# Optimization experiments

Measured on AMD Instinct MI355X. Metric: run time of the kernel, lower is better.

The kernel has to match this reference:

```python
import jax, jax.numpy as jnp
import numpy as np

B, C, H, W, K = 8, 512, 64, 64, 3
EPS = 1e-8


def setup_inputs() -> dict:
    key = jax.random.key(0)
    ks = jax.random.split(key, 7)
    return {
        "x": jax.random.normal(ks[0], (B, C, H, W), jnp.float32),
        "w": jax.random.normal(ks[1], (B, C), jnp.float32),
        "noise": jax.random.normal(ks[2], (B, 1, H, W), jnp.float32),
        # learned params (randn init as in the torch module)
        "conv_weight": jax.random.normal(ks[3], (C, C, K, K), jnp.float32),   # [out_ch, in_ch, k, k]
        "style_weight": jax.random.normal(ks[4], (C, C), jnp.float32),        # EqualizedLinear weight
        "style_bias": jnp.zeros((C,), jnp.float32),
        "bias": jax.random.normal(ks[5], (C,), jnp.float32),
        "scale_noise": jax.random.normal(ks[6], (1,), jnp.float32),
    }


def reference(x, w, noise, conv_weight, style_weight, style_bias, bias, scale_noise):
    b, c, h, wd = x.shape
    c_style = 1.0 / np.sqrt(C)          # EqualizedWeights c for [C, C]
    c_conv = 1.0 / np.sqrt(C * K * K)   # EqualizedWeights c for [C, C, K, K]

    # style vector s: equalized linear
    s = w @ (style_weight * c_style).T + style_bias            # [B, C]

    # per-sample modulation of input channels, demodulation per output channel
    wmod = (conv_weight * c_conv)[None] * s[:, None, :, None, None]   # [B, O, I, K, K]
    demod = jax.lax.rsqrt(jnp.sum(wmod * wmod, axis=(2, 3, 4), keepdims=True) + EPS)
    wmod = wmod * demod

    # grouped conv: fold batch into channels, one group per sample
    xg = x.reshape(1, b * c, h, wd)
    wg = wmod.reshape(b * C, C, K, K)
    y = jax.lax.conv_general_dilated(
        xg, wg, window_strides=(1, 1), padding="SAME",
        feature_group_count=b, dimension_numbers=("NCHW", "OIHW", "NCHW"))
    y = y.reshape(b, C, h, wd)

    # noise + bias + LeakyReLU(0.2)
    y = y + scale_noise[None, :, None, None] * noise
    return jax.nn.leaky_relu(y + bias[None, :, None, None], negative_slope=0.2)
```

## Files before the change

### kernel.cpp

```cpp
#include <hip/hip_runtime.h>


#define CC 512
#define BB 8
#define HWSZ 4096

#define C_STYLE 0.04419417382415922f
#define C_CONV  0.014731391274719739f

typedef __attribute__((ext_vector_type(8))) short bf16x8;
typedef __attribute__((ext_vector_type(4))) float f32x4;

static __device__ __forceinline__ short f2bf(float f) {
  unsigned u = __float_as_uint(f);
  unsigned r = (u + 0x7fffu + ((u >> 16) & 1u)) >> 16;
  return (short)r;
}

static __device__ __forceinline__ void load_lds_16(const void* g, void* l) {
  __builtin_amdgcn_global_load_lds(
      (const __attribute__((address_space(1))) unsigned int*)g,
      (__attribute__((address_space(3))) unsigned int*)l, 16, 0, 0);
}

__global__ __launch_bounds__(256) void prepA_kernel(
    const float* __restrict__ w,
    const float* __restrict__ sw,
    const float* __restrict__ sbias,
    float* __restrict__ alpha,
    const float* __restrict__ cw,
    short* __restrict__ wfrag,
    float* __restrict__ wsq) {
  __shared__ float lds[16][288];
  if (blockIdx.x < 1024) {
    int wv = (blockIdx.x * blockDim.x + threadIdx.x) >> 6;
    int lane = threadIdx.x & 63;
    int b = wv >> 9;
    int j = wv & 511;
    float acc = 0.f;
    const float* wr = w + b * CC;
    const float* sr = sw + (size_t)j * CC;
#pragma unroll
    for (int k = 0; k < CC; k += 64) acc = fmaf(wr[k + lane], sr[k + lane], acc);
#pragma unroll
    for (int off = 32; off > 0; off >>= 1) acc += __shfl_down(acc, off);
    if (lane == 0) alpha[wv] = C_CONV * fmaf(C_STYLE, acc, sbias[j]);
  } else {
    const int bid = blockIdx.x - 1024;
    const int ob = bid & 31;
    const int ib32 = bid >> 5;
    const int tid = threadIdx.x;
    const int o0 = ob * 16;
    const float* src = cw + (size_t)o0 * 4608 + ib32 * 288;
#pragma unroll
    for (int k = 0; k < 18; ++k) {
      int idx = k * 256 + tid;
      int row = idx / 288;
      int col = idx - row * 288;
      lds[row][col] = src[(size_t)row * 4608 + col];
    }
    __syncthreads();
#pragma unroll
    for (int pp = 0; pp < 2; ++pp) {
      int p = pp * 256 + tid;
      int row = p >> 5;
      int il = p & 31;
      float s = 0.f;
#pragma unroll
      for (int t9 = 0; t9 < 9; ++t9) {
        float v = lds[row][il * 9 + t9];
        s = fmaf(v, v, s);
      }
      wsq[(size_t)(o0 + row) * 512 + ib32 * 32 + il] = s;
    }
    const int lane = tid >> 2;
    const int jj = (tid & 3) * 2;
    const int row = lane & 15;
    const int ilb = ((lane >> 4) & 3) * 8 + jj;
    short* dst = wfrag + ((size_t)ib32 * 32 + ob) * 512 + tid * 2;
#pragma unroll
    for (int t9 = 0; t9 < 9; ++t9) {
      short2 v;
      v.x = f2bf(lds[row][ilb * 9 + t9]);
      v.y = f2bf(lds[row][(ilb + 1) * 9 + t9]);
      *(short2*)(dst + (size_t)t9 * 16 * 32 * 512) = v;
    }
  }
}

__global__ void prepB_kernel(const float* __restrict__ alpha,
                             const float* __restrict__ wsq,
                             float* __restrict__ demod,
                             const float* __restrict__ x,
                             short* __restrict__ xT) {
  if (blockIdx.x < 1024) {
    int wv = (blockIdx.x * blockDim.x + threadIdx.x) >> 6;
    int lane = threadIdx.x & 63;
    int b = wv >> 9;
    int o = wv & 511;
    const float* ar = alpha + b * CC;
    const float* qr = wsq + (size_t)o * CC;
    float s = 0.f;
#pragma unroll
    for (int i = 0; i < CC; i += 64) {
      float a = ar[i + lane];
      s = fmaf(a * a, qr[i + lane], s);
    }
#pragma unroll
    for (int off = 32; off > 0; off >>= 1) s += __shfl_down(s, off);
    if (lane == 0) {
      s += 1e-8f;
      float r = rsqrtf(s);
      r = r * fmaf(-0.5f * s * r, r, 1.5f);
      demod[wv] = r;
    }
  } else {
    const int id = blockIdx.x - 1024;
    const int py = id % 66;
    const int rem = id / 66;
    const int icg = rem & 15;
    const int b = rem >> 4;
    const int ic = icg * 4 + (threadIdx.x >> 6);
    const int px = threadIdx.x & 63;
    bf16x8 v = (bf16x8){0, 0, 0, 0, 0, 0, 0, 0};
    if (py >= 1 && py <= 64) {
      const float* xp =
          x + (((size_t)b * CC + ic * 8) * HWSZ + (py - 1) * 64 + px);
      const float* al = alpha + b * CC + ic * 8;
#pragma unroll
      for (int j = 0; j < 8; ++j) v[j] = f2bf(xp[(size_t)j * HWSZ] * al[j]);
    }
    short* row = xT + (((size_t)(b * 64 + ic) * 66 + py) * 66) * 8;
    *(bf16x8*)(row + (px + 1) * 8) = v;
    bf16x8 z = (bf16x8){0, 0, 0, 0, 0, 0, 0, 0};
    if (px == 0) *(bf16x8*)(row) = z;
    if (px == 63) *(bf16x8*)(row + 65 * 8) = z;
  }
}

#define NCHUNK 2112
__global__ __launch_bounds__(256, 2) void conv_kernel(
    const short* __restrict__ xT,
    const short* __restrict__ wfrag,
    const float* __restrict__ noise,
    const float* __restrict__ bias,
    const float* __restrict__ scale_noise,
    const float* __restrict__ demod,
    float* __restrict__ out) {
  __shared__ __align__(16) short xs[NCHUNK * 8];

  const int lin = blockIdx.x + 32 * blockIdx.y + 64 * blockIdx.z;
  const int xcd = lin & 7;
  const int j = lin >> 3;
  const int G = xcd & 1;
  const int b = (xcd >> 1) + 4 * (j & 1);
  const int y0 = (j >> 1) * 2;
  const int tid = threadIdx.x;
  const int lane = tid & 63;
  const int wave = tid >> 6;
  const int n = lane & 15;
  const int quad = lane >> 4;

  f32x4 acc[4][8];
#pragma unroll
  for (int p = 0; p < 4; ++p)
#pragma unroll
    for (int q = 0; q < 8; ++q) acc[p][q] = (f32x4){0.f, 0.f, 0.f, 0.f};

  const char* xTb = (const char*)xT;
  unsigned goff[9];
#pragma unroll
  for (int it = 0; it < 9; ++it) {
    int cid = tid + it * 256;
    int kc = cid / 264;
    int rem = cid - kc * 264;
    int r = rem / 66;
    int c = rem - r * 66;
    goff[it] = (unsigned)((((b * 64 + kc) * 66 + (y0 + r)) * 66 + c) * 16);
  }

  const short* wf0 = wfrag + ((size_t)((G * 16 + wave * 4) * 64 + lane)) * 8;

  for (int ib = 0; ib < 8; ++ib) {
    __syncthreads();
#pragma unroll
    for (int it = 0; it < 9; ++it) {
      int cid = tid + it * 256;
      if (cid < NCHUNK)
        load_lds_16(xTb + goff[it], xs + (size_t)cid * 8);
      goff[it] += 8 * 66 * 66 * 16;
    }
    __syncthreads();

#pragma unroll
    for (int kstep = 0; kstep < 2; ++kstep) {
      const int ib32 = ib * 2 + kstep;
#pragma unroll
      for (int t = 0; t < 9; ++t) {
        const int dy = t / 3 - 1;
        const int dx = t % 3 - 1;
        const short* wp = wf0 + (size_t)(t * 16 + ib32) * 16384;
        bf16x8 af[4];
#pragma unroll
        for (int p = 0; p < 4; ++p)
          af[p] = *(const bf16x8*)(wp + p * 512);
        const short* bp =
            xs + (((kstep * 4 + quad) * 4 + dy + 1) * 66 + 1 + n + dx) * 8;
        bf16x8 bf[8];
#pragma unroll
        for (int q = 0; q < 8; ++q)
          bf[q] = *(const bf16x8*)(bp + ((q >> 2) * 66 + (q & 3) * 16) * 8);
        __builtin_amdgcn_s_setprio(1);
#pragma unroll
        for (int p = 0; p < 4; ++p)
#pragma unroll
          for (int q = 0; q < 8; ++q)
            acc[p][q] = __builtin_amdgcn_mfma_f32_16x16x32_bf16(
                af[p], bf[q], acc[p][q], 0, 0, 0);
        __builtin_amdgcn_s_setprio(0);
      }
    }
  }

  const float sn = scale_noise[0];
#pragma unroll
  for (int q = 0; q < 8; ++q) {
    const int y = y0 + (q >> 2);
    const int col = (q & 3) * 16 + n;
    const float nz = sn * noise[b * HWSZ + y * 64 + col];
#pragma unroll
    for (int p = 0; p < 4; ++p) {
      const int o0 = G * 256 + wave * 64 + p * 16 + quad * 4;
#pragma unroll
      for (int r = 0; r < 4; ++r) {
        const int o = o0 + r;
        float v = fmaf(acc[p][q][r], demod[b * CC + o], nz + bias[o]);
        out[((size_t)(b * CC + o)) * HWSZ + y * 64 + col] =
            v > 0.f ? v : 0.2f * v;
      }
    }
  }
}

extern "C" void kernel_launch(void* const* d_in, const int* in_sizes, int n_in,
                              void* d_out, int out_size, void* d_ws, size_t ws_size,
                              hipStream_t stream) {
  const float* x     = (const float*)d_in[0];
  const float* w     = (const float*)d_in[1];
  const float* noise = (const float*)d_in[2];
  const float* cw    = (const float*)d_in[3];
  const float* sw    = (const float*)d_in[4];
  const float* sbias = (const float*)d_in[5];
  const float* bias  = (const float*)d_in[6];
  const float* sn    = (const float*)d_in[7];
  float* out = (float*)d_out;

  float* alpha = (float*)d_ws;
  float* demod = alpha + BB * CC;
  float* wsq   = demod + BB * CC;
  short* wfrag = (short*)(wsq + CC * CC);
  short* xT    = wfrag + (size_t)9 * 16 * 32 * 64 * 8;

  prepA_kernel<<<dim3(1024 + 512), 256, 0, stream>>>(
      w, sw, sbias, alpha, cw, wfrag, wsq);
  prepB_kernel<<<dim3(1024 + 66 * 16 * BB), 256, 0, stream>>>(
      alpha, wsq, demod, x, xT);
  conv_kernel<<<dim3(32, 2, BB), 256, 0, stream>>>(
      xT, wfrag, noise, bias, sn, demod, out);
}
```

Before: 248.3 us.

## Double-buffer conv LDS tiles and enlarge blocks to four output rows

The conv kernel now uses 512-thread blocks covering four output rows. Pairs of waves share the same output-channel slice but handle different row pairs, so each weight fragment load feeds twice as much input. The input halo tile is double-buffered in LDS, with the next input-channel slice prefetched via global_load_lds during compute, replacing the load-then-sync pattern. The relative halo overhead also drops from 4 to 6 rows per 2 to 4 output rows. In exchange, LDS use per block grows to about 100KB and there are half as many blocks (256), which may reduce occupancy.

```diff
diff --git a/kernel.cpp b/kernel.cpp
--- a/kernel.cpp
+++ b/kernel.cpp
@@ -138,8 +138,8 @@
   }
 }
 
-#define NCHUNK 2112
-__global__ __launch_bounds__(256, 2) void conv_kernel(
+#define NCHUNK6 3168
+__global__ __launch_bounds__(512, 2) void conv_kernel(
     const short* __restrict__ xT,
     const short* __restrict__ wfrag,
     const float* __restrict__ noise,
@@ -147,17 +147,19 @@
     const float* __restrict__ scale_noise,
     const float* __restrict__ demod,
     float* __restrict__ out) {
-  __shared__ __align__(16) short xs[NCHUNK * 8];
-
-  const int lin = blockIdx.x + 32 * blockIdx.y + 64 * blockIdx.z;
+  __shared__ __align__(16) short xs[2 * NCHUNK6 * 8];
+
+  const int lin = blockIdx.x + 32 * blockIdx.y;
   const int xcd = lin & 7;
   const int j = lin >> 3;
   const int G = xcd & 1;
   const int b = (xcd >> 1) + 4 * (j & 1);
-  const int y0 = (j >> 1) * 2;
+  const int y0 = (j >> 1) * 4;
   const int tid = threadIdx.x;
   const int lane = tid & 63;
   const int wave = tid >> 6;
+  const int ow = wave >> 1;
+  const int pw = wave & 1;
   const int n = lane & 15;
   const int quad = lane >> 4;
 
@@ -168,29 +170,29 @@
     for (int q = 0; q < 8; ++q) acc[p][q] = (f32x4){0.f, 0.f, 0.f, 0.f};
 
   const char* xTb = (const char*)xT;
-  unsigned goff[9];
-#pragma unroll
-  for (int it = 0; it < 9; ++it) {
-    int cid = tid + it * 256;
-    int kc = cid / 264;
-    int rem = cid - kc * 264;
+  unsigned goff[7];
+#pragma unroll
+  for (int it = 0; it < 7; ++it) {
+    int cid = tid + it * 512;
+    int kc = cid / 396;
+    int rem = cid - kc * 396;
     int r = rem / 66;
     int c = rem - r * 66;
     goff[it] = (unsigned)((((b * 64 + kc) * 66 + (y0 + r)) * 66 + c) * 16);
   }
 
-  const short* wf0 = wfrag + ((size_t)((G * 16 + wave * 4) * 64 + lane)) * 8;
+  const short* wf0 = wfrag + ((size_t)((G * 16 + ow * 4) * 64 + lane)) * 8;
+
+#pragma unroll
+  for (int it = 0; it < 7; ++it) {
+    int cid = tid + it * 512;
+    if (cid < NCHUNK6) load_lds_16(xTb + goff[it], xs + (size_t)cid * 8);
+    goff[it] += 8 * 66 * 66 * 16;
+  }
 
   for (int ib = 0; ib < 8; ++ib) {
     __syncthreads();
-#pragma unroll
-    for (int it = 0; it < 9; ++it) {
-      int cid = tid + it * 256;
-      if (cid < NCHUNK)
-        load_lds_16(xTb + goff[it], xs + (size_t)cid * 8);
-      goff[it] += 8 * 66 * 66 * 16;
-    }
-    __syncthreads();
+    const short* cxs = xs + (size_t)(ib & 1) * NCHUNK6 * 8;
 
 #pragma unroll
     for (int kstep = 0; kstep < 2; ++kstep) {
@@ -204,8 +206,19 @@
 #pragma unroll
         for (int p = 0; p < 4; ++p)
           af[p] = *(const bf16x8*)(wp + p * 512);
+        if (kstep == 0 && t == 1 && ib < 7) {
+#pragma unroll
+          for (int it = 0; it < 7; ++it) {
+            int cid = tid + it * 512;
+            if (cid < NCHUNK6)
+              load_lds_16(xTb + goff[it],
+                          xs + (size_t)(((ib & 1) ^ 1) * NCHUNK6 + cid) * 8);
+            goff[it] += 8 * 66 * 66 * 16;
+          }
+        }
+        const int row = pw * 2 + dy + 1;
         const short* bp =
-            xs + (((kstep * 4 + quad) * 4 + dy + 1) * 66 + 1 + n + dx) * 8;
+            cxs + (((kstep * 4 + quad) * 6 + row) * 66 + 1 + n + dx) * 8;
         bf16x8 bf[8];
 #pragma unroll
         for (int q = 0; q < 8; ++q)
@@ -225,12 +238,12 @@
   const float sn = scale_noise[0];
 #pragma unroll
   for (int q = 0; q < 8; ++q) {
-    const int y = y0 + (q >> 2);
+    const int y = y0 + pw * 2 + (q >> 2);
     const int col = (q & 3) * 16 + n;
     const float nz = sn * noise[b * HWSZ + y * 64 + col];
 #pragma unroll
     for (int p = 0; p < 4; ++p) {
-      const int o0 = G * 256 + wave * 64 + p * 16 + quad * 4;
+      const int o0 = G * 256 + ow * 64 + p * 16 + quad * 4;
 #pragma unroll
       for (int r = 0; r < 4; ++r) {
         const int o = o0 + r;
@@ -265,6 +278,6 @@
       w, sw, sbias, alpha, cw, wfrag, wsq);
   prepB_kernel<<<dim3(1024 + 66 * 16 * BB), 256, 0, stream>>>(
       alpha, wsq, demod, x, xT);
-  conv_kernel<<<dim3(32, 2, BB), 256, 0, stream>>>(
+  conv_kernel<<<dim3(32, 8), 512, 0, stream>>>(
       xT, wfrag, noise, bias, sn, demod, out);
 }
```

Result: no change. 244.7 us (-1.5%).
